# Kernel tuning notes

Hardware: AMD Instinct MI355X
Metric: run time of the kernel (lower is better)

Reference implementation:

```python
import jax, jax.numpy as jnp
import numpy as np

K = 5  # kernel_size
PAD = K // 2


def _median_filter(x):
    # x: [B,1,H,W]; reflect pad then 5x5 window median (lower median of 25 elems == true median)
    B, C, H, W = x.shape
    xp = jnp.pad(x, ((0, 0), (0, 0), (PAD, PAD), (PAD, PAD)), mode='reflect')
    windows = jnp.stack([xp[:, :, dy:dy + H, dx:dx + W]
                         for dy in range(K) for dx in range(K)], axis=0)
    return jnp.median(windows, axis=0)


def _gaussian_kernel(sigma):
    c = K // 2
    coords = jnp.arange(K, dtype=jnp.float32) - c
    d2 = coords[:, None] ** 2 + coords[None, :] ** 2  # [K,K]
    kern = jnp.exp(-d2 / (2.0 * sigma ** 2)) / (2.0 * jnp.pi * sigma ** 2)
    kern = kern / kern.sum()
    return kern[None, None]  # [1,1,K,K] (OIHW, single channel, groups=1)


def setup_inputs() -> dict:
    key = jax.random.key(0)
    img = jax.random.normal(key, (8, 1024, 1024), dtype=jnp.float32)
    sigma = jnp.float32(4.0)  # learnable parameter of the Gaussian filter
    return {"img": img, "sigma": sigma}


def reference(img, sigma):
    x = img[:, None]           # [B,1,H,W]
    x = _median_filter(x)      # [B,1,H,W]
    kern = _gaussian_kernel(sigma)
    x = jax.lax.conv_general_dilated(
        x, kern, window_strides=(1, 1),
        padding=[(PAD, PAD), (PAD, PAD)],
        dimension_numbers=('NCHW', 'OIHW', 'NCHW'))
    return x[:, 0]             # [B,H,W]
```

## Files before the change

kernel.cpp:

```cpp
#include <hip/hip_runtime.h>

#define HH 1024
#define WW 1024
#define NIMG 8
#define TROWS 16
#define NSTEP (TROWS + 4)

__device__ __forceinline__ float med3f(float a, float b, float c) {
    return __builtin_amdgcn_fmed3f(a, b, c);
}
__device__ __forceinline__ float min3f(float a, float b, float c) {
    return fminf(fminf(a, b), c);
}
__device__ __forceinline__ float max3f(float a, float b, float c) {
    return fmaxf(fmaxf(a, b), c);
}

__device__ __forceinline__ void top2(float a, float b, float c, float d, float e,
                                     float& r3, float& r4) {
    float m3 = med3f(a, b, c);
    float h3 = max3f(a, b, c);
    float s2 = med3f(m3, h3, d);
    float s3 = fmaxf(h3, d);
    r3 = med3f(s2, s3, e);
    r4 = fmaxf(s3, e);
}
__device__ __forceinline__ void bot2(float a, float b, float c, float d, float e,
                                     float& r0, float& r1) {
    float l3 = min3f(a, b, c);
    float m3 = med3f(a, b, c);
    float s0 = fminf(l3, d);
    float s1 = med3f(l3, m3, d);
    r0 = fminf(s0, e);
    r1 = med3f(s0, s1, e);
}
__device__ __forceinline__ void top3(float a, float b, float c, float d, float e,
                                     float& r2, float& r3, float& r4) {
    float l3 = min3f(a, b, c);
    float m3 = med3f(a, b, c);
    float h3 = max3f(a, b, c);
    float s1 = med3f(l3, m3, d);
    float s2 = med3f(m3, h3, d);
    float s3 = fmaxf(h3, d);
    r2 = med3f(s1, s2, e);
    r3 = med3f(s2, s3, e);
    r4 = fmaxf(s3, e);
}
__device__ __forceinline__ void bot3(float a, float b, float c, float d, float e,
                                     float& r0, float& r1, float& r2) {
    float l3 = min3f(a, b, c);
    float m3 = med3f(a, b, c);
    float h3 = max3f(a, b, c);
    float s0 = fminf(l3, d);
    float s1 = med3f(l3, m3, d);
    float s2 = med3f(m3, h3, d);
    r0 = fminf(s0, e);
    r1 = med3f(s0, s1, e);
    r2 = med3f(s1, s2, e);
}
__device__ __forceinline__ void mid3(float a, float b, float c, float d, float e,
                                     float& r1, float& r2, float& r3) {
    float l3 = min3f(a, b, c);
    float m3 = med3f(a, b, c);
    float h3 = max3f(a, b, c);
    float s0 = fminf(l3, d);
    float s1 = med3f(l3, m3, d);
    float s2 = med3f(m3, h3, d);
    float s3 = fmaxf(h3, d);
    r1 = med3f(s0, s1, e);
    r2 = med3f(s1, s2, e);
    r3 = med3f(s2, s3, e);
}

__device__ __forceinline__ void loadrow(const float* __restrict__ base, int r,
                                        int tid, int x0, float (&d)[8]) {
    const int rr = (r < 0) ? -r : (r >= HH ? 2 * HH - 2 - r : r);
    const float* rp = base + (size_t)rr * WW;
    const float4 A = *reinterpret_cast<const float4*>(rp + (tid == 0   ? x0 : x0 - 4));
    const float4 B = *reinterpret_cast<const float4*>(rp + x0);
    const float4 C = *reinterpret_cast<const float4*>(rp + (tid == 255 ? x0 : x0 + 4));
    d[0] = (tid == 0)   ? B.z : A.z;
    d[1] = (tid == 0)   ? B.y : A.w;
    d[2] = B.x; d[3] = B.y; d[4] = B.z; d[5] = B.w;
    d[6] = (tid == 255) ? B.z : C.x;
    d[7] = (tid == 255) ? B.y : C.y;
}

__device__ __forceinline__ void med4net(const float (&S0)[8], const float (&S1)[8],
                                        const float (&S2)[8], const float (&S3)[8],
                                        const float (&S4)[8], float (&med)[4]) {
    #pragma unroll
    for (int j = 0; j < 4; ++j) {
        float r03, r04, r12, r13, r14, r21, r22, r23, r30, r31, r32, r40, r41;
        top2(S0[j], S0[j+1], S0[j+2], S0[j+3], S0[j+4], r03, r04);
        top3(S1[j], S1[j+1], S1[j+2], S1[j+3], S1[j+4], r12, r13, r14);
        mid3(S2[j], S2[j+1], S2[j+2], S2[j+3], S2[j+4], r21, r22, r23);
        bot3(S3[j], S3[j+1], S3[j+2], S3[j+3], S3[j+4], r30, r31, r32);
        bot2(S4[j], S4[j+1], S4[j+2], S4[j+3], S4[j+4], r40, r41);
        float u = fminf(r40, r31), v = fmaxf(r40, r31);
        float w = fminf(v, r32),  x = fmaxf(v, r32);
        float ps0 = r30, ps1 = u, ps2 = w;
        float ps3 = fminf(x, r41), ps4 = fmaxf(x, r41);
        float q0 = fminf(r21, r03);
        float q1 = med3f(r21, r22, r03);
        float q2 = med3f(r22, r23, r03);
        float t1 = fminf(q1, r04);
        float t2 = med3f(q1, q2, r04);
        float t3 = med3f(q2, r23, r04);
        float t4 = fmaxf(r23, r04);
        float Y0 = fmaxf(ps0, q0);
        float Y1 = fmaxf(ps1, t1);
        float X2 = fminf(ps2, t2), Y2 = fmaxf(ps2, t2);
        float X3 = fminf(ps3, t3);
        float X4 = fminf(ps4, t4);
        float L  = max3f(X2, Y0, r12);
        float M  = med3f(X3, Y1, r13);
        float Hc = min3f(X4, Y2, r14);
        med[j] = med3f(L, M, Hc);
    }
}

template<int K>
__device__ __forceinline__ void dstep(int y0, int tid, int x0,
                                      const float* __restrict__ base,
                                      float* __restrict__ obase,
                                      const float (&wv)[5],
                                      float (&ring)[8][8], float (&hr)[6][4],
                                      float (*lbuf)[1032]) {
    float ha[8], hb[8];
    if constexpr (K >= 1) {
        const float* La = lbuf[2 * ((K + 1) & 1)];
        const float* Lb = lbuf[2 * ((K + 1) & 1) + 1];
        const float4 a0 = *reinterpret_cast<const float4*>(&La[x0]);
        const float4 a1 = *reinterpret_cast<const float4*>(&La[x0 + 4]);
        const float4 b0 = *reinterpret_cast<const float4*>(&Lb[x0]);
        const float4 b1 = *reinterpret_cast<const float4*>(&Lb[x0 + 4]);
        ha[0]=a0.x; ha[1]=a0.y; ha[2]=a0.z; ha[3]=a0.w;
        ha[4]=a1.x; ha[5]=a1.y; ha[6]=a1.z; ha[7]=a1.w;
        hb[0]=b0.x; hb[1]=b0.y; hb[2]=b0.z; hb[3]=b0.w;
        hb[4]=b1.x; hb[5]=b1.y; hb[6]=b1.z; hb[7]=b1.w;
    }
    if constexpr (K <= 8) {
        loadrow(base, y0 + 2 + 2 * K, tid, x0, ring[(2 * K + 6) & 7]);
        loadrow(base, y0 + 3 + 2 * K, tid, x0, ring[(2 * K + 7) & 7]);
    }
    if constexpr (K <= 9) {
        constexpr int s0 = (2*K) & 7,     s1 = (2*K + 1) & 7, s2 = (2*K + 2) & 7;
        constexpr int s3 = (2*K + 3) & 7, s4 = (2*K + 4) & 7, s5 = (2*K + 5) & 7;
        float T0[8], T1[8], T2[8], T3[8];
        #pragma unroll
        for (int c = 0; c < 8; ++c) {
            float b = ring[s1][c], cc = ring[s2][c], d = ring[s3][c], e = ring[s4][c];
            float l3 = min3f(b, cc, d);
            float m3 = med3f(b, cc, d);
            float h3 = max3f(b, cc, d);
            T0[c] = fminf(l3, e);
            T1[c] = med3f(l3, m3, e);
            T2[c] = med3f(m3, h3, e);
            T3[c] = fmaxf(h3, e);
        }
        const int m0 = y0 - 2 + 2 * K;
        float med0[4] = {0.f, 0.f, 0.f, 0.f};
        float med1[4] = {0.f, 0.f, 0.f, 0.f};
        if (m0 >= 0 && m0 < HH) {
            float S0[8], S1[8], S2[8], S3[8], S4[8];
            #pragma unroll
            for (int c = 0; c < 8; ++c) {
                float a = ring[s0][c];
                S0[c] = fminf(T0[c], a);
                S1[c] = med3f(T0[c], T1[c], a);
                S2[c] = med3f(T1[c], T2[c], a);
                S3[c] = med3f(T2[c], T3[c], a);
                S4[c] = fmaxf(T3[c], a);
            }
            med4net(S0, S1, S2, S3, S4, med0);
        }
        const int m1 = m0 + 1;
        if (m1 >= 0 && m1 < HH) {
            float S0[8], S1[8], S2[8], S3[8], S4[8];
            #pragma unroll
            for (int c = 0; c < 8; ++c) {
                float f = ring[s5][c];
                S0[c] = fminf(T0[c], f);
                S1[c] = med3f(T0[c], T1[c], f);
                S2[c] = med3f(T1[c], T2[c], f);
                S3[c] = med3f(T2[c], T3[c], f);
                S4[c] = fmaxf(T3[c], f);
            }
            med4net(S0, S1, S2, S3, S4, med1);
        }
        float* Lw0 = lbuf[2 * (K & 1)];
        float* Lw1 = lbuf[2 * (K & 1) + 1];
        *reinterpret_cast<float2*>(&Lw0[x0 + 2]) = make_float2(med0[0], med0[1]);
        *reinterpret_cast<float2*>(&Lw0[x0 + 4]) = make_float2(med0[2], med0[3]);
        *reinterpret_cast<float2*>(&Lw1[x0 + 2]) = make_float2(med1[0], med1[1]);
        *reinterpret_cast<float2*>(&Lw1[x0 + 4]) = make_float2(med1[2], med1[3]);
    }
    if constexpr (K >= 1) {
        #pragma unroll
        for (int j = 0; j < 4; ++j) {
            float h = 0.f;
            #pragma unroll
            for (int c = 0; c < 5; ++c) h = fmaf(wv[c], ha[j + c], h);
            hr[(2 * K) % 6][j] = h;
        }
        #pragma unroll
        for (int j = 0; j < 4; ++j) {
            float h = 0.f;
            #pragma unroll
            for (int c = 0; c < 5; ++c) h = fmaf(wv[c], hb[j + c], h);
            hr[(2 * K + 1) % 6][j] = h;
        }
    }
    if constexpr (K >= 3) {
        {
            float a0 = 0.f, a1 = 0.f, a2 = 0.f, a3 = 0.f;
            #pragma unroll
            for (int k = 0; k < 5; ++k) {
                const int   sl = (2 * K - 4 + k) % 6;
                const float wy = wv[k];
                a0 = fmaf(wy, hr[sl][0], a0);
                a1 = fmaf(wy, hr[sl][1], a1);
                a2 = fmaf(wy, hr[sl][2], a2);
                a3 = fmaf(wy, hr[sl][3], a3);
            }
            const int o0 = y0 - 6 + 2 * K;
            *reinterpret_cast<float4*>(obase + (size_t)o0 * WW + x0) =
                make_float4(a0, a1, a2, a3);
        }
        {
            float a0 = 0.f, a1 = 0.f, a2 = 0.f, a3 = 0.f;
            #pragma unroll
            for (int k = 0; k < 5; ++k) {
                const int   sl = (2 * K - 3 + k) % 6;
                const float wy = wv[k];
                a0 = fmaf(wy, hr[sl][0], a0);
                a1 = fmaf(wy, hr[sl][1], a1);
                a2 = fmaf(wy, hr[sl][2], a2);
                a3 = fmaf(wy, hr[sl][3], a3);
            }
            const int o1 = y0 - 5 + 2 * K;
            *reinterpret_cast<float4*>(obase + (size_t)o1 * WW + x0) =
                make_float4(a0, a1, a2, a3);
        }
    }
    if constexpr (K < 10) __syncthreads();
}

__global__ __launch_bounds__(256, 2) void fused_kernel(const float* __restrict__ in,
                                                       const float* __restrict__ sig,
                                                       float* __restrict__ out) {
    const int bi   = blockIdx.x;
    const int img  = bi & 7;
    const int tile = bi >> 3;
    const int y0   = tile * TROWS;
    const int tid  = threadIdx.x;
    const int x0   = tid * 4;
    const float* base  = in  + (size_t)img * HH * WW;
    float*       obase = out + (size_t)img * HH * WW;

    const float sigma  = sig[0];
    const float inv2s2 = 1.0f / (2.0f * sigma * sigma);
    const float g1 = expf(-1.0f * inv2s2);
    const float g4 = expf(-4.0f * inv2s2);
    const float sn = 1.0f + 2.0f * g1 + 2.0f * g4;
    const float wv[5] = { g4 / sn, g1 / sn, 1.0f / sn, g1 / sn, g4 / sn };

    __shared__ float lbuf[4][1032];
    if (tid < 8) {
        const int r = tid >> 1, p = tid & 1;
        lbuf[r][p] = 0.f;
        lbuf[r][1026 + p] = 0.f;
    }

    float ring[8][8];
    float hr[6][4];

    #pragma unroll
    for (int k = 0; k < 6; ++k) loadrow(base, y0 - 4 + k, tid, x0, ring[k]);

    dstep<0>(y0, tid, x0, base, obase, wv, ring, hr, lbuf);
    dstep<1>(y0, tid, x0, base, obase, wv, ring, hr, lbuf);
    dstep<2>(y0, tid, x0, base, obase, wv, ring, hr, lbuf);
    dstep<3>(y0, tid, x0, base, obase, wv, ring, hr, lbuf);
    dstep<4>(y0, tid, x0, base, obase, wv, ring, hr, lbuf);
    dstep<5>(y0, tid, x0, base, obase, wv, ring, hr, lbuf);
    dstep<6>(y0, tid, x0, base, obase, wv, ring, hr, lbuf);
    dstep<7>(y0, tid, x0, base, obase, wv, ring, hr, lbuf);
    dstep<8>(y0, tid, x0, base, obase, wv, ring, hr, lbuf);
    dstep<9>(y0, tid, x0, base, obase, wv, ring, hr, lbuf);
    dstep<10>(y0, tid, x0, base, obase, wv, ring, hr, lbuf);
}

extern "C" void kernel_launch(void* const* d_in, const int* in_sizes, int n_in,
                              void* d_out, int out_size, void* d_ws, size_t ws_size,
                              hipStream_t stream) {
    const float* img = (const float*)d_in[0];
    const float* sig = (const float*)d_in[1];
    float* out = (float*)d_out;

    dim3 grid(NIMG * (HH / TROWS));
    dim3 block(256);
    hipLaunchKernelGGL(fused_kernel, grid, block, 0, stream, img, sig, out);
}
```

Baseline: 37.41 us.

## Batch median rows in registers and exchange halos via wave shuffles

Replaces the per-step LDS row buffer and the eleven block-wide barriers with register storage of ten median rows per batch. Horizontal neighbours now come from wave shuffles, and only the wave-edge seam values go through a small shared array, so just two barriers remain. This removes most LDS traffic and sync stalls. The cost is more register pressure from the medr array, which may hurt occupancy under launch bounds (256,2), and less overlap between the median and Gaussian stages.

```diff
diff --git a/kernel.cpp b/kernel.cpp
--- a/kernel.cpp
+++ b/kernel.cpp
@@ -4,7 +4,6 @@
 #define WW 1024
 #define NIMG 8
 #define TROWS 16
-#define NSTEP (TROWS + 4)
 
 __device__ __forceinline__ float med3f(float a, float b, float c) {
     return __builtin_amdgcn_fmed3f(a, b, c);
@@ -120,131 +119,125 @@
     }
 }
 
-template<int K>
-__device__ __forceinline__ void dstep(int y0, int tid, int x0,
-                                      const float* __restrict__ base,
-                                      float* __restrict__ obase,
-                                      const float (&wv)[5],
-                                      float (&ring)[8][8], float (&hr)[6][4],
-                                      float (*lbuf)[1032]) {
-    float ha[8], hb[8];
-    if constexpr (K >= 1) {
-        const float* La = lbuf[2 * ((K + 1) & 1)];
-        const float* Lb = lbuf[2 * ((K + 1) & 1) + 1];
-        const float4 a0 = *reinterpret_cast<const float4*>(&La[x0]);
-        const float4 a1 = *reinterpret_cast<const float4*>(&La[x0 + 4]);
-        const float4 b0 = *reinterpret_cast<const float4*>(&Lb[x0]);
-        const float4 b1 = *reinterpret_cast<const float4*>(&Lb[x0 + 4]);
-        ha[0]=a0.x; ha[1]=a0.y; ha[2]=a0.z; ha[3]=a0.w;
-        ha[4]=a1.x; ha[5]=a1.y; ha[6]=a1.z; ha[7]=a1.w;
-        hb[0]=b0.x; hb[1]=b0.y; hb[2]=b0.z; hb[3]=b0.w;
-        hb[4]=b1.x; hb[5]=b1.y; hb[6]=b1.z; hb[7]=b1.w;
-    }
-    if constexpr (K <= 8) {
-        loadrow(base, y0 + 2 + 2 * K, tid, x0, ring[(2 * K + 6) & 7]);
-        loadrow(base, y0 + 3 + 2 * K, tid, x0, ring[(2 * K + 7) & 7]);
-    }
-    if constexpr (K <= 9) {
-        constexpr int s0 = (2*K) & 7,     s1 = (2*K + 1) & 7, s2 = (2*K + 2) & 7;
-        constexpr int s3 = (2*K + 3) & 7, s4 = (2*K + 4) & 7, s5 = (2*K + 5) & 7;
-        float T0[8], T1[8], T2[8], T3[8];
+template<int P>
+__device__ __forceinline__ void pairstep(int y0, int tid, int x0, int lane, int w,
+                                         const float* __restrict__ base,
+                                         float (&ring)[8][8], float (&medr)[10][4],
+                                         float (*seam)[4][10][4]) {
+    constexpr int B  = P / 5;
+    constexpr int RR = 2 * (P % 5);
+    if constexpr (P <= 8) {
+        loadrow(base, y0 + 2 + 2 * P, tid, x0, ring[(2 * P + 6) & 7]);
+        loadrow(base, y0 + 3 + 2 * P, tid, x0, ring[(2 * P + 7) & 7]);
+    }
+    constexpr int s0 = (2*P) & 7,     s1 = (2*P + 1) & 7, s2 = (2*P + 2) & 7;
+    constexpr int s3 = (2*P + 3) & 7, s4 = (2*P + 4) & 7, s5 = (2*P + 5) & 7;
+    float T0[8], T1[8], T2[8], T3[8];
+    #pragma unroll
+    for (int c = 0; c < 8; ++c) {
+        float b = ring[s1][c], cc = ring[s2][c], d = ring[s3][c], e = ring[s4][c];
+        float l3 = min3f(b, cc, d);
+        float m3 = med3f(b, cc, d);
+        float h3 = max3f(b, cc, d);
+        T0[c] = fminf(l3, e);
+        T1[c] = med3f(l3, m3, e);
+        T2[c] = med3f(m3, h3, e);
+        T3[c] = fmaxf(h3, e);
+    }
+    const int m0 = y0 - 2 + 2 * P;
+    float med0[4] = {0.f, 0.f, 0.f, 0.f};
+    float med1[4] = {0.f, 0.f, 0.f, 0.f};
+    if (m0 >= 0 && m0 < HH) {
+        float S0[8], S1[8], S2[8], S3[8], S4[8];
         #pragma unroll
         for (int c = 0; c < 8; ++c) {
-            float b = ring[s1][c], cc = ring[s2][c], d = ring[s3][c], e = ring[s4][c];
-            float l3 = min3f(b, cc, d);
-            float m3 = med3f(b, cc, d);
-            float h3 = max3f(b, cc, d);
-            T0[c] = fminf(l3, e);
-            T1[c] = med3f(l3, m3, e);
-            T2[c] = med3f(m3, h3, e);
-            T3[c] = fmaxf(h3, e);
-        }
-        const int m0 = y0 - 2 + 2 * K;
-        float med0[4] = {0.f, 0.f, 0.f, 0.f};
-        float med1[4] = {0.f, 0.f, 0.f, 0.f};
-        if (m0 >= 0 && m0 < HH) {
-            float S0[8], S1[8], S2[8], S3[8], S4[8];
-            #pragma unroll
-            for (int c = 0; c < 8; ++c) {
-                float a = ring[s0][c];
-                S0[c] = fminf(T0[c], a);
-                S1[c] = med3f(T0[c], T1[c], a);
-                S2[c] = med3f(T1[c], T2[c], a);
-                S3[c] = med3f(T2[c], T3[c], a);
-                S4[c] = fmaxf(T3[c], a);
-            }
-            med4net(S0, S1, S2, S3, S4, med0);
-        }
-        const int m1 = m0 + 1;
-        if (m1 >= 0 && m1 < HH) {
-            float S0[8], S1[8], S2[8], S3[8], S4[8];
-            #pragma unroll
-            for (int c = 0; c < 8; ++c) {
-                float f = ring[s5][c];
-                S0[c] = fminf(T0[c], f);
-                S1[c] = med3f(T0[c], T1[c], f);
-                S2[c] = med3f(T1[c], T2[c], f);
-                S3[c] = med3f(T2[c], T3[c], f);
-                S4[c] = fmaxf(T3[c], f);
-            }
-            med4net(S0, S1, S2, S3, S4, med1);
-        }
-        float* Lw0 = lbuf[2 * (K & 1)];
-        float* Lw1 = lbuf[2 * (K & 1) + 1];
-        *reinterpret_cast<float2*>(&Lw0[x0 + 2]) = make_float2(med0[0], med0[1]);
-        *reinterpret_cast<float2*>(&Lw0[x0 + 4]) = make_float2(med0[2], med0[3]);
-        *reinterpret_cast<float2*>(&Lw1[x0 + 2]) = make_float2(med1[0], med1[1]);
-        *reinterpret_cast<float2*>(&Lw1[x0 + 4]) = make_float2(med1[2], med1[3]);
-    }
-    if constexpr (K >= 1) {
+            float a = ring[s0][c];
+            S0[c] = fminf(T0[c], a);
+            S1[c] = med3f(T0[c], T1[c], a);
+            S2[c] = med3f(T1[c], T2[c], a);
+            S3[c] = med3f(T2[c], T3[c], a);
+            S4[c] = fmaxf(T3[c], a);
+        }
+        med4net(S0, S1, S2, S3, S4, med0);
+    }
+    if (m0 + 1 >= 0 && m0 + 1 < HH) {
+        float S0[8], S1[8], S2[8], S3[8], S4[8];
+        #pragma unroll
+        for (int c = 0; c < 8; ++c) {
+            float f = ring[s5][c];
+            S0[c] = fminf(T0[c], f);
+            S1[c] = med3f(T0[c], T1[c], f);
+            S2[c] = med3f(T1[c], T2[c], f);
+            S3[c] = med3f(T2[c], T3[c], f);
+            S4[c] = fmaxf(T3[c], f);
+        }
+        med4net(S0, S1, S2, S3, S4, med1);
+    }
+    #pragma unroll
+    for (int j = 0; j < 4; ++j) { medr[RR][j] = med0[j]; medr[RR + 1][j] = med1[j]; }
+    if (lane == 0 || lane == 63) {
+        const int off = (lane == 0) ? 0 : 2;
+        float e00 = (lane == 0) ? med0[0] : med0[2];
+        float e01 = (lane == 0) ? med0[1] : med0[3];
+        float e10 = (lane == 0) ? med1[0] : med1[2];
+        float e11 = (lane == 0) ? med1[1] : med1[3];
+        *reinterpret_cast<float2*>(&seam[B][w][RR][off])     = make_float2(e00, e01);
+        *reinterpret_cast<float2*>(&seam[B][w][RR + 1][off]) = make_float2(e10, e11);
+    }
+}
+
+template<int B>
+__device__ __forceinline__ void gaussbatch(int y0, int x0, int lane, int w,
+                                           float* __restrict__ obase,
+                                           const float (&wv)[5],
+                                           const float (&medr)[10][4],
+                                           float (&hr)[6][4],
+                                           const float (*seam)[4][10][4]) {
+    #pragma unroll
+    for (int r = 0; r < 10; ++r) {
+        const int m = y0 - 2 + 10 * B + r;
+        const float m0 = medr[r][0], m1 = medr[r][1];
+        const float m2 = medr[r][2], m3 = medr[r][3];
+        float ml0 = __shfl_up(m2, 1);
+        float ml1 = __shfl_up(m3, 1);
+        float mr0 = __shfl_down(m0, 1);
+        float mr1 = __shfl_down(m1, 1);
+        if (lane == 0) {
+            if (w > 0) {
+                float2 t = *reinterpret_cast<const float2*>(&seam[B][w - 1][r][2]);
+                ml0 = t.x; ml1 = t.y;
+            } else { ml0 = 0.f; ml1 = 0.f; }
+        }
+        if (lane == 63) {
+            if (w < 3) {
+                float2 t = *reinterpret_cast<const float2*>(&seam[B][w + 1][r][0]);
+                mr0 = t.x; mr1 = t.y;
+            } else { mr0 = 0.f; mr1 = 0.f; }
+        }
+        const float hh[8] = { ml0, ml1, m0, m1, m2, m3, mr0, mr1 };
         #pragma unroll
         for (int j = 0; j < 4; ++j) {
             float h = 0.f;
             #pragma unroll
-            for (int c = 0; c < 5; ++c) h = fmaf(wv[c], ha[j + c], h);
-            hr[(2 * K) % 6][j] = h;
-        }
-        #pragma unroll
-        for (int j = 0; j < 4; ++j) {
-            float h = 0.f;
-            #pragma unroll
-            for (int c = 0; c < 5; ++c) h = fmaf(wv[c], hb[j + c], h);
-            hr[(2 * K + 1) % 6][j] = h;
-        }
-    }
-    if constexpr (K >= 3) {
-        {
+            for (int c = 0; c < 5; ++c) h = fmaf(wv[c], hh[j + c], h);
+            hr[(10 * B + r) % 6][j] = h;
+        }
+        if (10 * B + r >= 4) {
+            const int o = m - 2;
             float a0 = 0.f, a1 = 0.f, a2 = 0.f, a3 = 0.f;
             #pragma unroll
             for (int k = 0; k < 5; ++k) {
-                const int   sl = (2 * K - 4 + k) % 6;
+                const int   sl = (10 * B + r - 4 + k) % 6;
                 const float wy = wv[k];
                 a0 = fmaf(wy, hr[sl][0], a0);
                 a1 = fmaf(wy, hr[sl][1], a1);
                 a2 = fmaf(wy, hr[sl][2], a2);
                 a3 = fmaf(wy, hr[sl][3], a3);
             }
-            const int o0 = y0 - 6 + 2 * K;
-            *reinterpret_cast<float4*>(obase + (size_t)o0 * WW + x0) =
+            *reinterpret_cast<float4*>(obase + (size_t)o * WW + x0) =
                 make_float4(a0, a1, a2, a3);
         }
-        {
-            float a0 = 0.f, a1 = 0.f, a2 = 0.f, a3 = 0.f;
-            #pragma unroll
-            for (int k = 0; k < 5; ++k) {
-                const int   sl = (2 * K - 3 + k) % 6;
-                const float wy = wv[k];
-                a0 = fmaf(wy, hr[sl][0], a0);
-                a1 = fmaf(wy, hr[sl][1], a1);
-                a2 = fmaf(wy, hr[sl][2], a2);
-                a3 = fmaf(wy, hr[sl][3], a3);
-            }
-            const int o1 = y0 - 5 + 2 * K;
-            *reinterpret_cast<float4*>(obase + (size_t)o1 * WW + x0) =
-                make_float4(a0, a1, a2, a3);
-        }
-    }
-    if constexpr (K < 10) __syncthreads();
+    }
 }
 
 __global__ __launch_bounds__(256, 2) void fused_kernel(const float* __restrict__ in,
@@ -256,6 +249,8 @@
     const int y0   = tile * TROWS;
     const int tid  = threadIdx.x;
     const int x0   = tid * 4;
+    const int lane = tid & 63;
+    const int w    = tid >> 6;
     const float* base  = in  + (size_t)img * HH * WW;
     float*       obase = out + (size_t)img * HH * WW;
 
@@ -266,30 +261,29 @@
     const float sn = 1.0f + 2.0f * g1 + 2.0f * g4;
     const float wv[5] = { g4 / sn, g1 / sn, 1.0f / sn, g1 / sn, g4 / sn };
 
-    __shared__ float lbuf[4][1032];
-    if (tid < 8) {
-        const int r = tid >> 1, p = tid & 1;
-        lbuf[r][p] = 0.f;
-        lbuf[r][1026 + p] = 0.f;
-    }
+    __shared__ float seam[2][4][10][4];
 
     float ring[8][8];
+    float medr[10][4];
     float hr[6][4];
 
     #pragma unroll
     for (int k = 0; k < 6; ++k) loadrow(base, y0 - 4 + k, tid, x0, ring[k]);
 
-    dstep<0>(y0, tid, x0, base, obase, wv, ring, hr, lbuf);
-    dstep<1>(y0, tid, x0, base, obase, wv, ring, hr, lbuf);
-    dstep<2>(y0, tid, x0, base, obase, wv, ring, hr, lbuf);
-    dstep<3>(y0, tid, x0, base, obase, wv, ring, hr, lbuf);
-    dstep<4>(y0, tid, x0, base, obase, wv, ring, hr, lbuf);
-    dstep<5>(y0, tid, x0, base, obase, wv, ring, hr, lbuf);
-    dstep<6>(y0, tid, x0, base, obase, wv, ring, hr, lbuf);
-    dstep<7>(y0, tid, x0, base, obase, wv, ring, hr, lbuf);
-    dstep<8>(y0, tid, x0, base, obase, wv, ring, hr, lbuf);
-    dstep<9>(y0, tid, x0, base, obase, wv, ring, hr, lbuf);
-    dstep<10>(y0, tid, x0, base, obase, wv, ring, hr, lbuf);
+    pairstep<0>(y0, tid, x0, lane, w, base, ring, medr, seam);
+    pairstep<1>(y0, tid, x0, lane, w, base, ring, medr, seam);
+    pairstep<2>(y0, tid, x0, lane, w, base, ring, medr, seam);
+    pairstep<3>(y0, tid, x0, lane, w, base, ring, medr, seam);
+    pairstep<4>(y0, tid, x0, lane, w, base, ring, medr, seam);
+    __syncthreads();
+    gaussbatch<0>(y0, x0, lane, w, obase, wv, medr, hr, seam);
+    pairstep<5>(y0, tid, x0, lane, w, base, ring, medr, seam);
+    pairstep<6>(y0, tid, x0, lane, w, base, ring, medr, seam);
+    pairstep<7>(y0, tid, x0, lane, w, base, ring, medr, seam);
+    pairstep<8>(y0, tid, x0, lane, w, base, ring, medr, seam);
+    pairstep<9>(y0, tid, x0, lane, w, base, ring, medr, seam);
+    __syncthreads();
+    gaussbatch<1>(y0, x0, lane, w, obase, wv, medr, hr, seam);
 }
 
 extern "C" void kernel_launch(void* const* d_in, const int* in_sizes, int n_in,
```

After: 38.65 us. +3.3%, slower.
